# Kernel optimization log

Hardware: AMD Instinct MI355X
Metric: run time of the kernel (lower is better)

Reference implementation:

```python
import jax, jax.numpy as jnp
import numpy as np
from jax import lax

FEAT_STRIDE = 16
BOX_SIZES = (4.0, 8.0, 12.0, 16.0, 24.0, 32.0, 48.0, 64.0, 96.0)
SCALE = 1.0
NUM_ANCHORS = 9
MIN_SIZE = 3.0          # rpn_config.MIN_SIZE (feature-map units)
NMS_THRESH = 0.7        # rpn_config.NMS_THRESH
PRE_NMS_TOP_N = 6000    # rpn_config.PRE_NMS_TOP_N
POST_NMS_TOP_N = 300    # rpn_config.POST_NMS_TOP_N


def _generate_anchors(H, W):
    # [A,H,W,4] boxes in (x, y, w, h); coord 0 pairs with the height axis,
    # matching clip_boxes_batch which clips index 0/2 against `length`=height.
    s = jnp.asarray(BOX_SIZES, jnp.float32) * SCALE                  # [A]
    cy = jnp.arange(H, dtype=jnp.float32) + 0.5
    cx = jnp.arange(W, dtype=jnp.float32) + 0.5
    shp = (NUM_ANCHORS, H, W)
    x0 = jnp.broadcast_to(cy[None, :, None] - s[:, None, None] / 2, shp)
    y0 = jnp.broadcast_to(cx[None, None, :] - s[:, None, None] / 2, shp)
    wh = jnp.broadcast_to(s[:, None, None], shp)
    return jnp.stack([x0, y0, wh, wh], axis=-1)


def _clip_boxes(boxes, H, W):
    # Faithful to clip_boxes_batch: clamp all entries at 0, convert to corners,
    # clamp x against height, y against width, convert back to (x,y,w,h).
    b = jnp.maximum(boxes, 0.0)
    x1, y1, w, h = b[..., 0], b[..., 1], b[..., 2], b[..., 3]
    x2, y2 = x1 + w, y1 + h
    x1 = jnp.minimum(x1, H)
    y1 = jnp.minimum(y1, W)
    x2 = jnp.minimum(x2, H)
    y2 = jnp.minimum(y2, W)
    return jnp.stack([x1, y1, x2 - x1, y2 - y1], axis=-1)


def setup_inputs() -> dict:
    key = jax.random.key(0)
    k1, k2 = jax.random.split(key)
    scores = jax.random.uniform(k1, (1, NUM_ANCHORS, 128, 128), dtype=jnp.float32)
    bbox_deltas = jax.random.normal(k2, (1, 4 * NUM_ANCHORS, 128, 128), dtype=jnp.float32)
    image_metadata = jnp.zeros((1, 3), dtype=jnp.float32)  # unused by forward
    return {"scores": scores, "bbox_deltas": bbox_deltas, "image_metadata": image_metadata}


def reference(scores, bbox_deltas, image_metadata):
    b, A, H, W = scores.shape
    anchors = _generate_anchors(H, W)[None]                 # [1,A,H,W,4]
    # torch view chain (A*4,H,W)->(A,4,H,W)->(A,H,W,4) over contiguous memory
    # is a single reshape of the flat buffer:
    deltas = bbox_deltas.reshape(b, A, H, W, 4)
    boxes = _clip_boxes(anchors + deltas, float(H), float(W))
    flat = boxes.reshape(-1, 4)                             # [N,4], N=A*H*W
    keep = (flat[:, 2] >= MIN_SIZE) & (flat[:, 3] >= MIN_SIZE)
    sc = jnp.where(keep, scores.reshape(-1), -jnp.inf)      # mask instead of compaction (jit-safe)
    _, top = lax.top_k(sc, PRE_NMS_TOP_N)                   # score-descending pre-NMS top-N
    props = flat[top]                                       # [K,4]

    # --- greedy NMS, processing order = descending y2 (as in source `nms`) ---
    x1, y1, w, h = props[:, 0], props[:, 1], props[:, 2], props[:, 3]
    x2, y2 = x1 + w, y1 + h
    order = jnp.argsort(-y2)
    x1, y1, x2, y2 = x1[order], y1[order], x2[order], y2[order]
    area = jnp.maximum((x2 - x1) * (y2 - y1), 1e-6)         # areas = l*b in source
    iw = jnp.maximum(jnp.minimum(x2[:, None], x2[None, :]) - jnp.maximum(x1[:, None], x1[None, :]) + 1.0, 0.0)
    ih = jnp.maximum(jnp.minimum(y2[:, None], y2[None, :]) - jnp.maximum(y1[:, None], y1[None, :]) + 1.0, 0.0)
    ov = iw * ih / area[None, :]                            # intersection / area[j], as in source

    K = PRE_NMS_TOP_N

    def body(valid, i):
        supp = (ov[i] >= NMS_THRESH) & valid
        supp = supp.at[i].set(False)
        return jnp.where(valid[i], valid & ~supp, valid), None

    valid, _ = lax.scan(body, jnp.ones((K,), bool), jnp.arange(K))

    # kept boxes first, in processing order; pad with zeros to POST_NMS_TOP_N
    perm = jnp.argsort(jnp.where(valid, jnp.arange(K), K))
    sel = perm[:POST_NMS_TOP_N]
    out = props[order][sel] * valid[sel][:, None].astype(props.dtype)
    return out[None]                                        # [1, POST_NMS_TOP_N, 4]
```

## Files before the change

### kernel.cpp

```cpp
#include <hip/hip_runtime.h>
#include <cstdint>
#include <cstddef>

#define N_TOT   147456
#define K_PRE   6000
#define K_POST  300
#define CAP     32768
#define MW      188
#define ROWS_PAD 6144
#define CH      256
#define NCH     24
#define CT      128
#define ROWB    24
#define COLB    47
#define G       16

__constant__ float c_sizes[9] = {4.f,8.f,12.f,16.f,24.f,32.f,48.f,64.f,96.f};

__device__ uint32_t g_hist[4096];
__device__ uint32_t g_cnt;

__device__ __forceinline__ void compute_box(int idx, const float* __restrict__ deltas,
                                            float& px1, float& py1, float& pw, float& ph) {
    int a   = idx >> 14;
    int rem = idx & 16383;
    int h   = rem >> 7;
    int w   = rem & 127;
    float s    = c_sizes[a];
    float half = s * 0.5f;
    const float4 d = *(const float4*)(deltas + (size_t)a * 65536 + (size_t)rem * 4);
    float b0 = (((float)h + 0.5f) - half) + d.x;
    float b1 = (((float)w + 0.5f) - half) + d.y;
    float b2 = s + d.z;
    float b3 = s + d.w;
    b0 = fmaxf(b0, 0.0f); b1 = fmaxf(b1, 0.0f);
    b2 = fmaxf(b2, 0.0f); b3 = fmaxf(b3, 0.0f);
    float x1 = b0, y1 = b1;
    float x2 = b0 + b2, y2 = b1 + b3;
    x1 = fminf(x1, 128.0f); y1 = fminf(y1, 128.0f);
    x2 = fminf(x2, 128.0f); y2 = fminf(y2, 128.0f);
    px1 = x1; py1 = y1; pw = x2 - x1; ph = y2 - y1;
}

__device__ __forceinline__ uint32_t waveReduceSum(uint32_t v) {
    #pragma unroll
    for (int o = 32; o > 0; o >>= 1) v += __shfl_xor(v, o, 64);
    return v;
}

__global__ void k_keys_hist(const float* __restrict__ scores, const float* __restrict__ deltas,
                            uint32_t* __restrict__ keys) {
    __shared__ uint32_t lh[4096];
    for (int i = threadIdx.x; i < 4096; i += 256) lh[i] = 0u;
    __syncthreads();
    int t4 = (blockIdx.x * 256 + threadIdx.x) * 4;
    float4 sc4 = *(const float4*)(scores + t4);
    uint32_t k4[4];
    #pragma unroll
    for (int e = 0; e < 4; e++) {
        int idx = t4 + e;
        float px1, py1, pw, ph;
        compute_box(idx, deltas, px1, py1, pw, ph);
        bool keep = (pw >= 3.0f) && (ph >= 3.0f);
        float sc = (&sc4.x)[e];
        uint32_t key = keep ? __float_as_uint(sc) : 0u;
        k4[e] = key;
        atomicAdd(&lh[key >> 20], 1u);
    }
    *(uint4*)(keys + t4) = make_uint4(k4[0], k4[1], k4[2], k4[3]);
    __syncthreads();
    for (int i = threadIdx.x; i < 4096; i += 256) {
        uint32_t v = lh[i];
        if (v) atomicAdd(&g_hist[i], v);
    }
}

__global__ void k_findbin_compact(const uint32_t* __restrict__ keys,
                                  uint64_t* __restrict__ cand) {
    __shared__ uint32_t lh[4096];
    __shared__ uint32_t seg[256];
    __shared__ uint32_t bsh;
    __shared__ uint32_t lcnt, lbase;
    if (threadIdx.x == 0) lcnt = 0u;
    for (int i = threadIdx.x; i < 4096; i += 256) lh[i] = g_hist[i];
    __syncthreads();
    uint32_t s = 0;
    #pragma unroll
    for (int q = 0; q < 16; q++) s += lh[threadIdx.x * 16 + q];
    seg[threadIdx.x] = s;
    __syncthreads();
    for (int off = 1; off < 256; off <<= 1) {
        uint32_t v = seg[threadIdx.x];
        if (threadIdx.x + off < 256) v += seg[threadIdx.x + off];
        __syncthreads();
        seg[threadIdx.x] = v;
        __syncthreads();
    }
    uint32_t St  = seg[threadIdx.x];
    uint32_t St1 = (threadIdx.x < 255) ? seg[threadIdx.x + 1] : 0u;
    if (St >= K_PRE && St1 < K_PRE) {
        uint32_t c2 = St1;
        uint32_t bstar = 0u;
        for (int q = 15; q >= 0; q--) {
            c2 += lh[threadIdx.x * 16 + q];
            if (c2 >= K_PRE) { bstar = (uint32_t)(threadIdx.x * 16 + q); break; }
        }
        bsh = bstar;
    }
    if (threadIdx.x == 0 && seg[0] < K_PRE) bsh = 0u;
    __syncthreads();
    uint32_t bstar = bsh;
    int t4 = (blockIdx.x * 256 + threadIdx.x) * 4;
    uint4 kk = *(const uint4*)(keys + t4);
    bool s0 = (kk.x >> 20) >= bstar;
    bool s1 = (kk.y >> 20) >= bstar;
    bool s2 = (kk.z >> 20) >= bstar;
    bool s3 = (kk.w >> 20) >= bstar;
    uint32_t nsel = (uint32_t)s0 + s1 + s2 + s3;
    uint32_t myoff = 0u;
    if (nsel) myoff = atomicAdd(&lcnt, nsel);
    __syncthreads();
    if (threadIdx.x == 0) lbase = atomicAdd(&g_cnt, lcnt);
    __syncthreads();
    uint32_t pos = lbase + myoff;
    if (s0) { if (pos < CAP) cand[pos] = ((uint64_t)kk.x << 32) | (uint32_t)(~(uint32_t)(t4 + 0)); pos++; }
    if (s1) { if (pos < CAP) cand[pos] = ((uint64_t)kk.y << 32) | (uint32_t)(~(uint32_t)(t4 + 1)); pos++; }
    if (s2) { if (pos < CAP) cand[pos] = ((uint64_t)kk.z << 32) | (uint32_t)(~(uint32_t)(t4 + 2)); pos++; }
    if (s3) { if (pos < CAP) cand[pos] = ((uint64_t)kk.w << 32) | (uint32_t)(~(uint32_t)(t4 + 3)); }
}

__global__ void __launch_bounds__(256) k_rank_props(
        const uint64_t* __restrict__ cand,
        const float* __restrict__ deltas,
        float4* __restrict__ P, uint64_t* __restrict__ yk) {
    __shared__ uint32_t part[4][G];
    uint32_t C = g_cnt;
    if (C > CAP) C = CAP;
    uint32_t nGroups = (C + G - 1) / G;
    int tid  = threadIdx.x;
    int wave = tid >> 6, lane = tid & 63;
    for (uint32_t g = blockIdx.x; g < nGroups; g += gridDim.x) {
        uint32_t b = g * G;
        uint64_t m[G];
        uint32_t cnt[G];
        #pragma unroll
        for (int q = 0; q < G; q++) {
            m[q] = (b + q < C) ? cand[b + q] : ~0ull;
            cnt[q] = 0u;
        }
        for (uint32_t j0 = 0; j0 < C; j0 += 1024) {
            uint32_t ja = j0 + tid, jb = ja + 256, jc = ja + 512, jd = ja + 768;
            uint64_t ka = (ja < C) ? cand[ja] : 0ull;
            uint64_t kb = (jb < C) ? cand[jb] : 0ull;
            uint64_t kc = (jc < C) ? cand[jc] : 0ull;
            uint64_t kd = (jd < C) ? cand[jd] : 0ull;
            #pragma unroll
            for (int q = 0; q < G; q++)
                cnt[q] += (uint32_t)(ka > m[q]) + (uint32_t)(kb > m[q])
                        + (uint32_t)(kc > m[q]) + (uint32_t)(kd > m[q]);
        }
        #pragma unroll
        for (int q = 0; q < G; q++) cnt[q] = waveReduceSum(cnt[q]);
        if (lane == 0) {
            #pragma unroll
            for (int q = 0; q < G; q++) part[wave][q] = cnt[q];
        }
        __syncthreads();
        if (tid < G && b + tid < C) {
            uint32_t r = part[0][tid] + part[1][tid] + part[2][tid] + part[3][tid];
            if (r < K_PRE) {
                int idx = (int)(~((uint32_t)cand[b + tid]));
                float px1, py1, pw, ph;
                compute_box(idx, deltas, px1, py1, pw, ph);
                P[r] = make_float4(px1, py1, pw, ph);
                float y2 = py1 + ph;
                yk[r] = ((uint64_t)__float_as_uint(y2) << 32) | (uint32_t)(~r);
            }
        }
        __syncthreads();
    }
}

__global__ void __launch_bounds__(256) k_rank_y2(
        const uint64_t* __restrict__ ykey, const float4* __restrict__ P,
        float4* __restrict__ OP, float4* __restrict__ Q, float* __restrict__ Bnd) {
    __shared__ uint32_t part[4][G];
    int tid  = threadIdx.x;
    int wave = tid >> 6, lane = tid & 63;
    uint32_t b = blockIdx.x * G;
    uint64_t m[G];
    uint32_t cnt[G];
    #pragma unroll
    for (int q = 0; q < G; q++) {
        m[q] = ykey[b + q];
        cnt[q] = 0u;
    }
    for (uint32_t j0 = 0; j0 < K_PRE; j0 += 1024) {
        uint32_t ja = j0 + tid, jb = ja + 256, jc = ja + 512, jd = ja + 768;
        uint64_t ka = (ja < K_PRE) ? ykey[ja] : 0ull;
        uint64_t kb = (jb < K_PRE) ? ykey[jb] : 0ull;
        uint64_t kc = (jc < K_PRE) ? ykey[jc] : 0ull;
        uint64_t kd = (jd < K_PRE) ? ykey[jd] : 0ull;
        #pragma unroll
        for (int q = 0; q < G; q++)
            cnt[q] += (uint32_t)(ka > m[q]) + (uint32_t)(kb > m[q])
                    + (uint32_t)(kc > m[q]) + (uint32_t)(kd > m[q]);
    }
    #pragma unroll
    for (int q = 0; q < G; q++) cnt[q] = waveReduceSum(cnt[q]);
    if (lane == 0) {
        #pragma unroll
        for (int q = 0; q < G; q++) part[wave][q] = cnt[q];
    }
    __syncthreads();
    if (tid < G) {
        uint32_t r = part[0][tid] + part[1][tid] + part[2][tid] + part[3][tid];
        float4 p = P[b + tid];
        OP[r] = p;
        float x1 = p.x, y1 = p.y;
        float x2 = x1 + p.z, y2 = y1 + p.w;
        float area = fmaxf((x2 - x1) * (y2 - y1), 1e-6f);
        Q[r] = make_float4(x1, y1, x2, y2);
        const double Mc = (double)0.7f - 0x1.0p-25;
        double c = Mc * (double)area;
        float Bf = (float)c;
        if (!((double)Bf > c)) Bf = __int_as_float(__float_as_int(Bf) + 1);
        Bnd[r] = Bf;
    }
}

__global__ void __launch_bounds__(256) k_mask(const float4* __restrict__ Q,
                                              const float* __restrict__ Bnd,
                                              uint32_t* __restrict__ mask) {
    __shared__ float4 qs[CT];
    __shared__ float  bs[CT];
    int i  = blockIdx.x * 256 + threadIdx.x;
    int c0 = blockIdx.y * CT;
    int ncols = min(CT, K_PRE - c0);
    bool rowok = (i < K_PRE);
    float4 qi = rowok ? Q[i] : make_float4(0.f, 0.f, 0.f, 0.f);
    for (int j = threadIdx.x; j < ncols; j += 256) {
        qs[j] = Q[c0 + j];
        bs[j] = Bnd[c0 + j];
    }
    __syncthreads();
    int nw = (ncols + 31) >> 5;
    for (int w = 0; w < nw; w++) {
        uint32_t bits = 0u;
        int jb = w * 32;
        int jn = min(32, ncols - jb);
        #pragma unroll 8
        for (int b = 0; b < jn; b++) {
            int j = jb + b;
            float4 qj = qs[j];
            float iw = fminf(qi.z, qj.z) - fmaxf(qi.x, qj.x) + 1.0f;
            iw = fmaxf(iw, 0.0f);
            float ih = fminf(qi.w, qj.w) - fmaxf(qi.y, qj.y) + 1.0f;
            ih = fmaxf(ih, 0.0f);
            float d = iw * ih;
            bits |= (d >= bs[j]) ? (1u << b) : 0u;
        }
        if (rowok) {
            int gj = c0 + jb;
            uint32_t selfo = (uint32_t)(i - gj);
            if (selfo < 32u) bits &= ~(1u << selfo);
            mask[(size_t)i * MW + (gj >> 5)] = bits;
        }
    }
}

__global__ void __launch_bounds__(256) k_scan(const uint32_t* __restrict__ mask,
                                              const float4* __restrict__ OP,
                                              float* __restrict__ out) {
    __shared__ uint32_t rem[192];
    __shared__ uint32_t sidx[CH];
    __shared__ uint32_t svL[192];
    __shared__ uint32_t nsSh;
    __shared__ uint32_t pref[MW];
    int tid = threadIdx.x;
    if (tid < 16) {
        #pragma unroll
        for (int q = 0; q < 16; q++) g_hist[tid * 16 + q] = 0u;
    }
    if (tid == 16) g_cnt = 0u;
    if (tid < 192) { rem[tid] = 0u; svL[tid] = 0u; }
    for (int i = tid; i < K_POST * 4; i += 256) out[i] = 0.0f;
    __syncthreads();
    uint4 s00 = make_uint4(0,0,0,0), s01 = s00, s10 = s00, s11 = s00;
    uint4 s20 = s00, s21 = s00, s30 = s00, s31 = s00;
    if (tid < 64) {
        const uint32_t* p0 = mask + (size_t)(tid) * MW;
        s00 = *(const uint4*)p0;       s01 = *(const uint4*)(p0 + 4);
        const uint32_t* p1 = mask + (size_t)(64 + tid) * MW;
        s10 = *(const uint4*)p1;       s11 = *(const uint4*)(p1 + 4);
        const uint32_t* p2 = mask + (size_t)(128 + tid) * MW;
        s20 = *(const uint4*)p2;       s21 = *(const uint4*)(p2 + 4);
        const uint32_t* p3 = mask + (size_t)(192 + tid) * MW;
        s30 = *(const uint4*)p3;       s31 = *(const uint4*)(p3 + 4);
    }
    for (int c = 0; c < NCH; c++) {
        int base = c * CH;
        if (tid < 64) {
            uint64_t w0 = ~(((uint64_t)rem[8*c+1] << 32) | (uint64_t)rem[8*c+0]);
            uint64_t w1 = ~(((uint64_t)rem[8*c+3] << 32) | (uint64_t)rem[8*c+2]);
            uint64_t w2 = ~(((uint64_t)rem[8*c+5] << 32) | (uint64_t)rem[8*c+4]);
            uint64_t w3 = ~(((uint64_t)rem[8*c+7] << 32) | (uint64_t)rem[8*c+6]);
            int rows = K_PRE - base;
            if (rows < CH) {
                auto msk = [](int v) -> uint64_t {
                    return v <= 0 ? 0ull : (v >= 64 ? ~0ull : ((1ull << v) - 1ull));
                };
                w0 &= msk(rows); w1 &= msk(rows - 64);
                w2 &= msk(rows - 128); w3 &= msk(rows - 192);
            }
            uint64_t sv0 = 0ull, sv1 = 0ull, sv2 = 0ull, sv3 = 0ull;
            while (w0 | w1 | w2 | w3) {
                int k;
                uint32_t a0, a1, a2, a3, a4, a5, a6, a7;
                if (w0) {
                    k = __ffsll((unsigned long long)w0) - 1;
                    sv0 |= 1ull << k; w0 &= ~(1ull << k);
                    a0 = (uint32_t)__builtin_amdgcn_readlane((int)s00.x, k);
                    a1 = (uint32_t)__builtin_amdgcn_readlane((int)s00.y, k);
                    a2 = (uint32_t)__builtin_amdgcn_readlane((int)s00.z, k);
                    a3 = (uint32_t)__builtin_amdgcn_readlane((int)s00.w, k);
                    a4 = (uint32_t)__builtin_amdgcn_readlane((int)s01.x, k);
                    a5 = (uint32_t)__builtin_amdgcn_readlane((int)s01.y, k);
                    a6 = (uint32_t)__builtin_amdgcn_readlane((int)s01.z, k);
                    a7 = (uint32_t)__builtin_amdgcn_readlane((int)s01.w, k);
                } else if (w1) {
                    k = __ffsll((unsigned long long)w1) - 1;
                    sv1 |= 1ull << k; w1 &= ~(1ull << k);
                    a0 = (uint32_t)__builtin_amdgcn_readlane((int)s10.x, k);
                    a1 = (uint32_t)__builtin_amdgcn_readlane((int)s10.y, k);
                    a2 = (uint32_t)__builtin_amdgcn_readlane((int)s10.z, k);
                    a3 = (uint32_t)__builtin_amdgcn_readlane((int)s10.w, k);
                    a4 = (uint32_t)__builtin_amdgcn_readlane((int)s11.x, k);
                    a5 = (uint32_t)__builtin_amdgcn_readlane((int)s11.y, k);
                    a6 = (uint32_t)__builtin_amdgcn_readlane((int)s11.z, k);
                    a7 = (uint32_t)__builtin_amdgcn_readlane((int)s11.w, k);
                } else if (w2) {
                    k = __ffsll((unsigned long long)w2) - 1;
                    sv2 |= 1ull << k; w2 &= ~(1ull << k);
                    a0 = (uint32_t)__builtin_amdgcn_readlane((int)s20.x, k);
                    a1 = (uint32_t)__builtin_amdgcn_readlane((int)s20.y, k);
                    a2 = (uint32_t)__builtin_amdgcn_readlane((int)s20.z, k);
                    a3 = (uint32_t)__builtin_amdgcn_readlane((int)s20.w, k);
                    a4 = (uint32_t)__builtin_amdgcn_readlane((int)s21.x, k);
                    a5 = (uint32_t)__builtin_amdgcn_readlane((int)s21.y, k);
                    a6 = (uint32_t)__builtin_amdgcn_readlane((int)s21.z, k);
                    a7 = (uint32_t)__builtin_amdgcn_readlane((int)s21.w, k);
                } else {
                    k = __ffsll((unsigned long long)w3) - 1;
                    sv3 |= 1ull << k; w3 &= ~(1ull << k);
                    a0 = (uint32_t)__builtin_amdgcn_readlane((int)s30.x, k);
                    a1 = (uint32_t)__builtin_amdgcn_readlane((int)s30.y, k);
                    a2 = (uint32_t)__builtin_amdgcn_readlane((int)s30.z, k);
                    a3 = (uint32_t)__builtin_amdgcn_readlane((int)s30.w, k);
                    a4 = (uint32_t)__builtin_amdgcn_readlane((int)s31.x, k);
                    a5 = (uint32_t)__builtin_amdgcn_readlane((int)s31.y, k);
                    a6 = (uint32_t)__builtin_amdgcn_readlane((int)s31.z, k);
                    a7 = (uint32_t)__builtin_amdgcn_readlane((int)s31.w, k);
                }
                w0 &= ~(((uint64_t)a1 << 32) | (uint64_t)a0);
                w1 &= ~(((uint64_t)a3 << 32) | (uint64_t)a2);
                w2 &= ~(((uint64_t)a5 << 32) | (uint64_t)a4);
                w3 &= ~(((uint64_t)a7 << 32) | (uint64_t)a6);
            }
            uint32_t n0 = (uint32_t)__popcll(sv0), n1 = (uint32_t)__popcll(sv1);
            uint32_t n2 = (uint32_t)__popcll(sv2), n3 = (uint32_t)__popcll(sv3);
            uint32_t o1 = n0, o2 = n0 + n1, o3 = n0 + n1 + n2, ns = o3 + n3;
            if (tid == 0) {
                svL[8*c+0] = (uint32_t)sv0; svL[8*c+1] = (uint32_t)(sv0 >> 32);
                svL[8*c+2] = (uint32_t)sv1; svL[8*c+3] = (uint32_t)(sv1 >> 32);
                svL[8*c+4] = (uint32_t)sv2; svL[8*c+5] = (uint32_t)(sv2 >> 32);
                svL[8*c+6] = (uint32_t)sv3; svL[8*c+7] = (uint32_t)(sv3 >> 32);
                nsSh = ns;
            }
            uint64_t lowm = (1ull << tid) - 1ull;
            if ((sv0 >> tid) & 1ull) sidx[      __popcll(sv0 & lowm)] = (uint32_t)(base + tid);
            if ((sv1 >> tid) & 1ull) sidx[o1 +  __popcll(sv1 & lowm)] = (uint32_t)(base + 64 + tid);
            if ((sv2 >> tid) & 1ull) sidx[o2 +  __popcll(sv2 & lowm)] = (uint32_t)(base + 128 + tid);
            if ((sv3 >> tid) & 1ull) sidx[o3 +  __popcll(sv3 & lowm)] = (uint32_t)(base + 192 + tid);
            if (ns) {
                uint32_t nsPad = (ns + 31u) & ~31u;
                uint32_t first;
                if      (sv0) first = (uint32_t)base +       (uint32_t)(__ffsll((unsigned long long)sv0) - 1);
                else if (sv1) first = (uint32_t)base + 64u + (uint32_t)(__ffsll((unsigned long long)sv1) - 1);
                else if (sv2) first = (uint32_t)base + 128u+ (uint32_t)(__ffsll((unsigned long long)sv2) - 1);
                else          first = (uint32_t)base + 192u+ (uint32_t)(__ffsll((unsigned long long)sv3) - 1);
                #pragma unroll
                for (int rr = 0; rr < 4; rr++) {
                    uint32_t ii = (uint32_t)tid + 64u * rr;
                    if (ii >= ns && ii < nsPad) sidx[ii] = first;
                }
            }
            if (c + 1 < NCH) {
                const uint32_t* p0 = mask + (size_t)(base + 256 + tid) * MW + 8*(c+1);
                s00 = *(const uint4*)p0;  s01 = *(const uint4*)(p0 + 4);
                const uint32_t* p1 = p0 + (size_t)64 * MW;
                s10 = *(const uint4*)p1;  s11 = *(const uint4*)(p1 + 4);
                const uint32_t* p2 = p1 + (size_t)64 * MW;
                s20 = *(const uint4*)p2;  s21 = *(const uint4*)(p2 + 4);
                const uint32_t* p3 = p2 + (size_t)64 * MW;
                s30 = *(const uint4*)p3;  s31 = *(const uint4*)(p3 + 4);
            }
        }
        __syncthreads();
        int w = tid - 64;
        if (w >= 0 && w < MW) {
            uint32_t nsPad = (nsSh + 31u) & ~31u;
            uint32_t acc = rem[w];
            for (uint32_t t2 = 0; t2 < nsPad; t2 += 32) {
                uint32_t r[32];
                #pragma unroll
                for (int q = 0; q < 32; q++)
                    r[q] = mask[(size_t)sidx[t2 + q] * MW + w];
                uint32_t o = 0u;
                #pragma unroll
                for (int q = 0; q < 32; q++) o |= r[q];
                acc |= o;
            }
            rem[w] = acc;
        }
        __syncthreads();
    }
    if (tid < MW) {
        uint32_t vv = svL[tid] & ~rem[tid];
        if (tid == MW - 1) vv &= 0xFFFFu;
        rem[tid] = vv;
    }
    __syncthreads();
    if (tid == 0) {
        uint32_t run = 0;
        for (int w2 = 0; w2 < MW; w2++) { pref[w2] = run; run += (uint32_t)__popc(rem[w2]); }
    }
    __syncthreads();
    if (tid < MW) {
        uint32_t b = rem[tid];
        uint32_t r = pref[tid];
        int basebit = tid * 32;
        while (b && r < K_POST) {
            int bit = __ffs(b) - 1;
            b &= b - 1u;
            float4 pp = OP[basebit + bit];
            *(float4*)(out + (size_t)r * 4) = pp;
            r++;
        }
    }
}

extern "C" void kernel_launch(void* const* d_in, const int* in_sizes, int n_in,
                              void* d_out, int out_size, void* d_ws, size_t ws_size,
                              hipStream_t stream) {
    (void)in_sizes; (void)n_in; (void)out_size; (void)ws_size;
    const float* scores = (const float*)d_in[0];
    const float* deltas = (const float*)d_in[1];
    float* out = (float*)d_out;

    char* ws = (char*)d_ws;
    size_t off = 0;
    auto alloc = [&](size_t bytes) -> void* {
        void* p = ws + off;
        off += (bytes + 255) & ~(size_t)255;
        return p;
    };
    uint32_t* keys  = (uint32_t*)alloc((size_t)N_TOT * 4);
    uint64_t* cand  = (uint64_t*)alloc((size_t)CAP * 8);
    float4*   P     = (float4*)alloc((size_t)K_PRE * 16);
    uint64_t* yk    = (uint64_t*)alloc((size_t)K_PRE * 8);
    float4*   OP    = (float4*)alloc((size_t)K_PRE * 16);
    float4*   Q     = (float4*)alloc((size_t)K_PRE * 16);
    float*    Bnd   = (float*)alloc((size_t)K_PRE * 4);
    uint32_t* mask  = (uint32_t*)alloc((size_t)ROWS_PAD * MW * 4 + 256);

    k_keys_hist<<<N_TOT / 1024, 256, 0, stream>>>(scores, deltas, keys);
    k_findbin_compact<<<N_TOT / 1024, 256, 0, stream>>>(keys, cand);
    k_rank_props<<<1024, 256, 0, stream>>>(cand, deltas, P, yk);
    k_rank_y2<<<K_PRE / G, 256, 0, stream>>>(yk, P, OP, Q, Bnd);
    k_mask<<<dim3(ROWB, COLB), 256, 0, stream>>>(Q, Bnd, mask);
    k_scan<<<1, 256, 0, stream>>>(mask, OP, out);
}
```

Measured before the change: 143.3 us.

## Fuse all six stages into one persistent kernel with grid barriers

Replaces the six separate kernel launches with a single persistent kernel of 576 blocks that runs histogram, compaction, score ranking, y2 ranking, mask building and the serial scan as phases separated by software grid barriers on global atomic counters. The goal is to remove per-launch overhead and the idle gaps between short dependent kernels. In exchange, it requires all 576 blocks to be co-resident, since the spin barriers would otherwise deadlock; the barrier loop has a timeout to guard against this. It also caps each block at 256 threads via launch bounds, and the final scan runs on one block while the others sit idle.

Result: slower. 405.1 us (+182.8%).

```diff
diff --git a/kernel.cpp b/kernel.cpp
--- a/kernel.cpp
+++ b/kernel.cpp
@@ -13,12 +13,42 @@
 #define CT      128
 #define ROWB    24
 #define COLB    47
+#define NTILE   (ROWB*COLB)
 #define G       16
+#define NBLK    576
+#define HBLK    144
+
+#define OFF_KEYS 0u
+#define OFF_CAND 589824u
+#define OFF_P    851968u
+#define OFF_YK   948224u
+#define OFF_OP   996352u
+#define OFF_Q    1092608u
+#define OFF_BND  1188864u
+#define OFF_MASK 1212928u
 
 __constant__ float c_sizes[9] = {4.f,8.f,12.f,16.f,24.f,32.f,48.f,64.f,96.f};
 
 __device__ uint32_t g_hist[4096];
 __device__ uint32_t g_cnt;
+__device__ uint32_t g_bar[8];
+
+__device__ __forceinline__ void gridBarrier(int i) {
+    __syncthreads();
+    if (threadIdx.x == 0) {
+        __threadfence();
+        uint32_t ticket = atomicAdd(&g_bar[i], 1u);
+        uint32_t target = (ticket / NBLK + 1u) * NBLK;
+        uint32_t tries = 0;
+        while (__hip_atomic_load(&g_bar[i], __ATOMIC_RELAXED,
+                                 __HIP_MEMORY_SCOPE_AGENT) < target) {
+            __builtin_amdgcn_s_sleep(2);
+            if (++tries > (1u << 24)) break;
+        }
+        __threadfence();
+    }
+    __syncthreads();
+}
 
 __device__ __forceinline__ void compute_box(int idx, const float* __restrict__ deltas,
                                             float& px1, float& py1, float& pw, float& ph) {
@@ -48,112 +78,171 @@
     return v;
 }
 
-__global__ void k_keys_hist(const float* __restrict__ scores, const float* __restrict__ deltas,
-                            uint32_t* __restrict__ keys) {
-    __shared__ uint32_t lh[4096];
-    for (int i = threadIdx.x; i < 4096; i += 256) lh[i] = 0u;
-    __syncthreads();
-    int t4 = (blockIdx.x * 256 + threadIdx.x) * 4;
-    float4 sc4 = *(const float4*)(scores + t4);
-    uint32_t k4[4];
-    #pragma unroll
-    for (int e = 0; e < 4; e++) {
-        int idx = t4 + e;
-        float px1, py1, pw, ph;
-        compute_box(idx, deltas, px1, py1, pw, ph);
-        bool keep = (pw >= 3.0f) && (ph >= 3.0f);
-        float sc = (&sc4.x)[e];
-        uint32_t key = keep ? __float_as_uint(sc) : 0u;
-        k4[e] = key;
-        atomicAdd(&lh[key >> 20], 1u);
-    }
-    *(uint4*)(keys + t4) = make_uint4(k4[0], k4[1], k4[2], k4[3]);
-    __syncthreads();
-    for (int i = threadIdx.x; i < 4096; i += 256) {
-        uint32_t v = lh[i];
-        if (v) atomicAdd(&g_hist[i], v);
-    }
-}
-
-__global__ void k_findbin_compact(const uint32_t* __restrict__ keys,
-                                  uint64_t* __restrict__ cand) {
-    __shared__ uint32_t lh[4096];
-    __shared__ uint32_t seg[256];
-    __shared__ uint32_t bsh;
-    __shared__ uint32_t lcnt, lbase;
-    if (threadIdx.x == 0) lcnt = 0u;
-    for (int i = threadIdx.x; i < 4096; i += 256) lh[i] = g_hist[i];
-    __syncthreads();
-    uint32_t s = 0;
-    #pragma unroll
-    for (int q = 0; q < 16; q++) s += lh[threadIdx.x * 16 + q];
-    seg[threadIdx.x] = s;
-    __syncthreads();
-    for (int off = 1; off < 256; off <<= 1) {
-        uint32_t v = seg[threadIdx.x];
-        if (threadIdx.x + off < 256) v += seg[threadIdx.x + off];
-        __syncthreads();
-        seg[threadIdx.x] = v;
-        __syncthreads();
-    }
-    uint32_t St  = seg[threadIdx.x];
-    uint32_t St1 = (threadIdx.x < 255) ? seg[threadIdx.x + 1] : 0u;
-    if (St >= K_PRE && St1 < K_PRE) {
-        uint32_t c2 = St1;
-        uint32_t bstar = 0u;
-        for (int q = 15; q >= 0; q--) {
-            c2 += lh[threadIdx.x * 16 + q];
-            if (c2 >= K_PRE) { bstar = (uint32_t)(threadIdx.x * 16 + q); break; }
-        }
-        bsh = bstar;
-    }
-    if (threadIdx.x == 0 && seg[0] < K_PRE) bsh = 0u;
-    __syncthreads();
-    uint32_t bstar = bsh;
-    int t4 = (blockIdx.x * 256 + threadIdx.x) * 4;
-    uint4 kk = *(const uint4*)(keys + t4);
-    bool s0 = (kk.x >> 20) >= bstar;
-    bool s1 = (kk.y >> 20) >= bstar;
-    bool s2 = (kk.z >> 20) >= bstar;
-    bool s3 = (kk.w >> 20) >= bstar;
-    uint32_t nsel = (uint32_t)s0 + s1 + s2 + s3;
-    uint32_t myoff = 0u;
-    if (nsel) myoff = atomicAdd(&lcnt, nsel);
-    __syncthreads();
-    if (threadIdx.x == 0) lbase = atomicAdd(&g_cnt, lcnt);
-    __syncthreads();
-    uint32_t pos = lbase + myoff;
-    if (s0) { if (pos < CAP) cand[pos] = ((uint64_t)kk.x << 32) | (uint32_t)(~(uint32_t)(t4 + 0)); pos++; }
-    if (s1) { if (pos < CAP) cand[pos] = ((uint64_t)kk.y << 32) | (uint32_t)(~(uint32_t)(t4 + 1)); pos++; }
-    if (s2) { if (pos < CAP) cand[pos] = ((uint64_t)kk.z << 32) | (uint32_t)(~(uint32_t)(t4 + 2)); pos++; }
-    if (s3) { if (pos < CAP) cand[pos] = ((uint64_t)kk.w << 32) | (uint32_t)(~(uint32_t)(t4 + 3)); }
-}
-
-__global__ void __launch_bounds__(256) k_rank_props(
-        const uint64_t* __restrict__ cand,
-        const float* __restrict__ deltas,
-        float4* __restrict__ P, uint64_t* __restrict__ yk) {
-    __shared__ uint32_t part[4][G];
-    uint32_t C = g_cnt;
-    if (C > CAP) C = CAP;
-    uint32_t nGroups = (C + G - 1) / G;
-    int tid  = threadIdx.x;
-    int wave = tid >> 6, lane = tid & 63;
-    for (uint32_t g = blockIdx.x; g < nGroups; g += gridDim.x) {
-        uint32_t b = g * G;
+__global__ void __launch_bounds__(256, 4) mega(const float* __restrict__ scores,
+                                               const float* __restrict__ deltas,
+                                               float* __restrict__ out,
+                                               char* __restrict__ ws) {
+    __shared__ __align__(16) char smem[17664];
+
+    uint32_t* keys = (uint32_t*)(ws + OFF_KEYS);
+    uint64_t* cand = (uint64_t*)(ws + OFF_CAND);
+    float4*   P    = (float4*)(ws + OFF_P);
+    uint64_t* yk   = (uint64_t*)(ws + OFF_YK);
+    float4*   OP   = (float4*)(ws + OFF_OP);
+    float4*   Q    = (float4*)(ws + OFF_Q);
+    float*    Bnd  = (float*)(ws + OFF_BND);
+    uint32_t* mask = (uint32_t*)(ws + OFF_MASK);
+
+    const int tid  = threadIdx.x;
+    const int bid  = blockIdx.x;
+    const int wave = tid >> 6, lane = tid & 63;
+
+    if (bid < HBLK) {
+        uint32_t* lh = (uint32_t*)smem;
+        for (int i = tid; i < 4096; i += 256) lh[i] = 0u;
+        __syncthreads();
+        int t4 = (bid * 256 + tid) * 4;
+        float4 sc4 = *(const float4*)(scores + t4);
+        uint32_t k4[4];
+        #pragma unroll
+        for (int e = 0; e < 4; e++) {
+            int idx = t4 + e;
+            float px1, py1, pw, ph;
+            compute_box(idx, deltas, px1, py1, pw, ph);
+            bool keep = (pw >= 3.0f) && (ph >= 3.0f);
+            float sc = (&sc4.x)[e];
+            uint32_t key = keep ? __float_as_uint(sc) : 0u;
+            k4[e] = key;
+            atomicAdd(&lh[key >> 20], 1u);
+        }
+        *(uint4*)(keys + t4) = make_uint4(k4[0], k4[1], k4[2], k4[3]);
+        __syncthreads();
+        for (int i = tid; i < 4096; i += 256) {
+            uint32_t v = lh[i];
+            if (v) atomicAdd(&g_hist[i], v);
+        }
+    }
+    gridBarrier(0);
+
+    if (bid < HBLK) {
+        uint32_t* lh   = (uint32_t*)smem;
+        uint32_t* seg  = (uint32_t*)(smem + 16384);
+        uint32_t* bshp = (uint32_t*)(smem + 16384 + 1024);
+        uint32_t* lcnt = bshp + 1;
+        uint32_t* lbas = bshp + 2;
+        if (tid == 0) lcnt[0] = 0u;
+        for (int i = tid; i < 4096; i += 256) lh[i] = g_hist[i];
+        __syncthreads();
+        uint32_t s = 0;
+        #pragma unroll
+        for (int q = 0; q < 16; q++) s += lh[tid * 16 + q];
+        seg[tid] = s;
+        __syncthreads();
+        for (int off = 1; off < 256; off <<= 1) {
+            uint32_t v = seg[tid];
+            if (tid + off < 256) v += seg[tid + off];
+            __syncthreads();
+            seg[tid] = v;
+            __syncthreads();
+        }
+        uint32_t St  = seg[tid];
+        uint32_t St1 = (tid < 255) ? seg[tid + 1] : 0u;
+        if (St >= K_PRE && St1 < K_PRE) {
+            uint32_t c2 = St1;
+            uint32_t bstar = 0u;
+            for (int q = 15; q >= 0; q--) {
+                c2 += lh[tid * 16 + q];
+                if (c2 >= K_PRE) { bstar = (uint32_t)(tid * 16 + q); break; }
+            }
+            bshp[0] = bstar;
+        }
+        if (tid == 0 && seg[0] < K_PRE) bshp[0] = 0u;
+        __syncthreads();
+        uint32_t bstar = bshp[0];
+        int t4 = (bid * 256 + tid) * 4;
+        uint4 kk = *(const uint4*)(keys + t4);
+        bool s0 = (kk.x >> 20) >= bstar;
+        bool s1 = (kk.y >> 20) >= bstar;
+        bool s2 = (kk.z >> 20) >= bstar;
+        bool s3 = (kk.w >> 20) >= bstar;
+        uint32_t nsel = (uint32_t)s0 + s1 + s2 + s3;
+        uint32_t myoff = 0u;
+        if (nsel) myoff = atomicAdd(lcnt, nsel);
+        __syncthreads();
+        if (tid == 0) lbas[0] = atomicAdd(&g_cnt, lcnt[0]);
+        __syncthreads();
+        uint32_t pos = lbas[0] + myoff;
+        if (s0) { if (pos < CAP) cand[pos] = ((uint64_t)kk.x << 32) | (uint32_t)(~(uint32_t)(t4 + 0)); pos++; }
+        if (s1) { if (pos < CAP) cand[pos] = ((uint64_t)kk.y << 32) | (uint32_t)(~(uint32_t)(t4 + 1)); pos++; }
+        if (s2) { if (pos < CAP) cand[pos] = ((uint64_t)kk.z << 32) | (uint32_t)(~(uint32_t)(t4 + 2)); pos++; }
+        if (s3) { if (pos < CAP) cand[pos] = ((uint64_t)kk.w << 32) | (uint32_t)(~(uint32_t)(t4 + 3)); }
+    }
+    gridBarrier(1);
+
+    {
+        uint32_t (*part)[G] = (uint32_t (*)[G])smem;
+        uint32_t C = g_cnt;
+        if (C > CAP) C = CAP;
+        uint32_t nGroups = (C + G - 1) / G;
+        for (uint32_t g = bid; g < nGroups; g += NBLK) {
+            uint32_t b = g * G;
+            uint64_t m[G];
+            uint32_t cnt[G];
+            #pragma unroll
+            for (int q = 0; q < G; q++) {
+                m[q] = (b + q < C) ? cand[b + q] : ~0ull;
+                cnt[q] = 0u;
+            }
+            for (uint32_t j0 = 0; j0 < C; j0 += 1024) {
+                uint32_t ja = j0 + tid, jb = ja + 256, jc = ja + 512, jd = ja + 768;
+                uint64_t ka = (ja < C) ? cand[ja] : 0ull;
+                uint64_t kb = (jb < C) ? cand[jb] : 0ull;
+                uint64_t kc = (jc < C) ? cand[jc] : 0ull;
+                uint64_t kd = (jd < C) ? cand[jd] : 0ull;
+                #pragma unroll
+                for (int q = 0; q < G; q++)
+                    cnt[q] += (uint32_t)(ka > m[q]) + (uint32_t)(kb > m[q])
+                            + (uint32_t)(kc > m[q]) + (uint32_t)(kd > m[q]);
+            }
+            #pragma unroll
+            for (int q = 0; q < G; q++) cnt[q] = waveReduceSum(cnt[q]);
+            if (lane == 0) {
+                #pragma unroll
+                for (int q = 0; q < G; q++) part[wave][q] = cnt[q];
+            }
+            __syncthreads();
+            if (tid < G && b + tid < C) {
+                uint32_t r = part[0][tid] + part[1][tid] + part[2][tid] + part[3][tid];
+                if (r < K_PRE) {
+                    int idx = (int)(~((uint32_t)cand[b + tid]));
+                    float px1, py1, pw, ph;
+                    compute_box(idx, deltas, px1, py1, pw, ph);
+                    P[r] = make_float4(px1, py1, pw, ph);
+                    float y2 = py1 + ph;
+                    yk[r] = ((uint64_t)__float_as_uint(y2) << 32) | (uint32_t)(~r);
+                }
+            }
+            __syncthreads();
+        }
+    }
+    gridBarrier(2);
+
+    if (bid < K_PRE / G) {
+        uint32_t (*part)[G] = (uint32_t (*)[G])smem;
+        uint32_t b = (uint32_t)bid * G;
         uint64_t m[G];
         uint32_t cnt[G];
         #pragma unroll
         for (int q = 0; q < G; q++) {
-            m[q] = (b + q < C) ? cand[b + q] : ~0ull;
+            m[q] = yk[b + q];
             cnt[q] = 0u;
         }
-        for (uint32_t j0 = 0; j0 < C; j0 += 1024) {
+        for (uint32_t j0 = 0; j0 < K_PRE; j0 += 1024) {
             uint32_t ja = j0 + tid, jb = ja + 256, jc = ja + 512, jd = ja + 768;
-            uint64_t ka = (ja < C) ? cand[ja] : 0ull;
-            uint64_t kb = (jb < C) ? cand[jb] : 0ull;
-            uint64_t kc = (jc < C) ? cand[jc] : 0ull;
-            uint64_t kd = (jd < C) ? cand[jd] : 0ull;
+            uint64_t ka = (ja < K_PRE) ? yk[ja] : 0ull;
+            uint64_t kb = (jb < K_PRE) ? yk[jb] : 0ull;
+            uint64_t kc = (jc < K_PRE) ? yk[jc] : 0ull;
+            uint64_t kd = (jd < K_PRE) ? yk[jd] : 0ull;
             #pragma unroll
             for (int q = 0; q < G; q++)
                 cnt[q] += (uint32_t)(ka > m[q]) + (uint32_t)(kb > m[q])
@@ -166,286 +255,243 @@
             for (int q = 0; q < G; q++) part[wave][q] = cnt[q];
         }
         __syncthreads();
-        if (tid < G && b + tid < C) {
+        if (tid < G) {
             uint32_t r = part[0][tid] + part[1][tid] + part[2][tid] + part[3][tid];
-            if (r < K_PRE) {
-                int idx = (int)(~((uint32_t)cand[b + tid]));
-                float px1, py1, pw, ph;
-                compute_box(idx, deltas, px1, py1, pw, ph);
-                P[r] = make_float4(px1, py1, pw, ph);
-                float y2 = py1 + ph;
-                yk[r] = ((uint64_t)__float_as_uint(y2) << 32) | (uint32_t)(~r);
-            }
-        }
-        __syncthreads();
-    }
-}
-
-__global__ void __launch_bounds__(256) k_rank_y2(
-        const uint64_t* __restrict__ ykey, const float4* __restrict__ P,
-        float4* __restrict__ OP, float4* __restrict__ Q, float* __restrict__ Bnd) {
-    __shared__ uint32_t part[4][G];
-    int tid  = threadIdx.x;
-    int wave = tid >> 6, lane = tid & 63;
-    uint32_t b = blockIdx.x * G;
-    uint64_t m[G];
-    uint32_t cnt[G];
-    #pragma unroll
-    for (int q = 0; q < G; q++) {
-        m[q] = ykey[b + q];
-        cnt[q] = 0u;
-    }
-    for (uint32_t j0 = 0; j0 < K_PRE; j0 += 1024) {
-        uint32_t ja = j0 + tid, jb = ja + 256, jc = ja + 512, jd = ja + 768;
-        uint64_t ka = (ja < K_PRE) ? ykey[ja] : 0ull;
-        uint64_t kb = (jb < K_PRE) ? ykey[jb] : 0ull;
-        uint64_t kc = (jc < K_PRE) ? ykey[jc] : 0ull;
-        uint64_t kd = (jd < K_PRE) ? ykey[jd] : 0ull;
-        #pragma unroll
-        for (int q = 0; q < G; q++)
-            cnt[q] += (uint32_t)(ka > m[q]) + (uint32_t)(kb > m[q])
-                    + (uint32_t)(kc > m[q]) + (uint32_t)(kd > m[q]);
-    }
-    #pragma unroll
-    for (int q = 0; q < G; q++) cnt[q] = waveReduceSum(cnt[q]);
-    if (lane == 0) {
-        #pragma unroll
-        for (int q = 0; q < G; q++) part[wave][q] = cnt[q];
-    }
-    __syncthreads();
-    if (tid < G) {
-        uint32_t r = part[0][tid] + part[1][tid] + part[2][tid] + part[3][tid];
-        float4 p = P[b + tid];
-        OP[r] = p;
-        float x1 = p.x, y1 = p.y;
-        float x2 = x1 + p.z, y2 = y1 + p.w;
-        float area = fmaxf((x2 - x1) * (y2 - y1), 1e-6f);
-        Q[r] = make_float4(x1, y1, x2, y2);
-        const double Mc = (double)0.7f - 0x1.0p-25;
-        double c = Mc * (double)area;
-        float Bf = (float)c;
-        if (!((double)Bf > c)) Bf = __int_as_float(__float_as_int(Bf) + 1);
-        Bnd[r] = Bf;
-    }
-}
-
-__global__ void __launch_bounds__(256) k_mask(const float4* __restrict__ Q,
-                                              const float* __restrict__ Bnd,
-                                              uint32_t* __restrict__ mask) {
-    __shared__ float4 qs[CT];
-    __shared__ float  bs[CT];
-    int i  = blockIdx.x * 256 + threadIdx.x;
-    int c0 = blockIdx.y * CT;
-    int ncols = min(CT, K_PRE - c0);
-    bool rowok = (i < K_PRE);
-    float4 qi = rowok ? Q[i] : make_float4(0.f, 0.f, 0.f, 0.f);
-    for (int j = threadIdx.x; j < ncols; j += 256) {
-        qs[j] = Q[c0 + j];
-        bs[j] = Bnd[c0 + j];
-    }
-    __syncthreads();
-    int nw = (ncols + 31) >> 5;
-    for (int w = 0; w < nw; w++) {
-        uint32_t bits = 0u;
-        int jb = w * 32;
-        int jn = min(32, ncols - jb);
-        #pragma unroll 8
-        for (int b = 0; b < jn; b++) {
-            int j = jb + b;
-            float4 qj = qs[j];
-            float iw = fminf(qi.z, qj.z) - fmaxf(qi.x, qj.x) + 1.0f;
-            iw = fmaxf(iw, 0.0f);
-            float ih = fminf(qi.w, qj.w) - fmaxf(qi.y, qj.y) + 1.0f;
-            ih = fmaxf(ih, 0.0f);
-            float d = iw * ih;
-            bits |= (d >= bs[j]) ? (1u << b) : 0u;
-        }
-        if (rowok) {
-            int gj = c0 + jb;
-            uint32_t selfo = (uint32_t)(i - gj);
-            if (selfo < 32u) bits &= ~(1u << selfo);
-            mask[(size_t)i * MW + (gj >> 5)] = bits;
-        }
-    }
-}
-
-__global__ void __launch_bounds__(256) k_scan(const uint32_t* __restrict__ mask,
-                                              const float4* __restrict__ OP,
-                                              float* __restrict__ out) {
-    __shared__ uint32_t rem[192];
-    __shared__ uint32_t sidx[CH];
-    __shared__ uint32_t svL[192];
-    __shared__ uint32_t nsSh;
-    __shared__ uint32_t pref[MW];
-    int tid = threadIdx.x;
-    if (tid < 16) {
-        #pragma unroll
-        for (int q = 0; q < 16; q++) g_hist[tid * 16 + q] = 0u;
-    }
-    if (tid == 16) g_cnt = 0u;
-    if (tid < 192) { rem[tid] = 0u; svL[tid] = 0u; }
-    for (int i = tid; i < K_POST * 4; i += 256) out[i] = 0.0f;
-    __syncthreads();
-    uint4 s00 = make_uint4(0,0,0,0), s01 = s00, s10 = s00, s11 = s00;
-    uint4 s20 = s00, s21 = s00, s30 = s00, s31 = s00;
-    if (tid < 64) {
-        const uint32_t* p0 = mask + (size_t)(tid) * MW;
-        s00 = *(const uint4*)p0;       s01 = *(const uint4*)(p0 + 4);
-        const uint32_t* p1 = mask + (size_t)(64 + tid) * MW;
-        s10 = *(const uint4*)p1;       s11 = *(const uint4*)(p1 + 4);
-        const uint32_t* p2 = mask + (size_t)(128 + tid) * MW;
-        s20 = *(const uint4*)p2;       s21 = *(const uint4*)(p2 + 4);
-        const uint32_t* p3 = mask + (size_t)(192 + tid) * MW;
-        s30 = *(const uint4*)p3;       s31 = *(const uint4*)(p3 + 4);
-    }
-    for (int c = 0; c < NCH; c++) {
-        int base = c * CH;
+            float4 p = P[b + tid];
+            OP[r] = p;
+            float x1 = p.x, y1 = p.y;
+            float x2 = x1 + p.z, y2 = y1 + p.w;
+            float area = fmaxf((x2 - x1) * (y2 - y1), 1e-6f);
+            Q[r] = make_float4(x1, y1, x2, y2);
+            const double Mc = (double)0.7f - 0x1.0p-25;
+            double c = Mc * (double)area;
+            float Bf = (float)c;
+            if (!((double)Bf > c)) Bf = __int_as_float(__float_as_int(Bf) + 1);
+            Bnd[r] = Bf;
+        }
+    }
+    gridBarrier(3);
+
+    {
+        float4* qs = (float4*)smem;
+        float*  bs = (float*)(smem + CT * 16);
+        for (uint32_t t = bid; t < NTILE; t += NBLK) {
+            int bx = (int)(t % ROWB);
+            int by = (int)(t / ROWB);
+            int i  = bx * 256 + tid;
+            int c0 = by * CT;
+            int ncols = min(CT, K_PRE - c0);
+            bool rowok = (i < K_PRE);
+            float4 qi = rowok ? Q[i] : make_float4(0.f, 0.f, 0.f, 0.f);
+            __syncthreads();
+            for (int j = tid; j < ncols; j += 256) {
+                qs[j] = Q[c0 + j];
+                bs[j] = Bnd[c0 + j];
+            }
+            __syncthreads();
+            int nw = (ncols + 31) >> 5;
+            for (int w = 0; w < nw; w++) {
+                uint32_t bits = 0u;
+                int jb = w * 32;
+                int jn = min(32, ncols - jb);
+                #pragma unroll 8
+                for (int b = 0; b < jn; b++) {
+                    int j = jb + b;
+                    float4 qj = qs[j];
+                    float iw = fminf(qi.z, qj.z) - fmaxf(qi.x, qj.x) + 1.0f;
+                    iw = fmaxf(iw, 0.0f);
+                    float ih = fminf(qi.w, qj.w) - fmaxf(qi.y, qj.y) + 1.0f;
+                    ih = fmaxf(ih, 0.0f);
+                    float d = iw * ih;
+                    bits |= (d >= bs[j]) ? (1u << b) : 0u;
+                }
+                if (rowok) {
+                    int gj = c0 + jb;
+                    uint32_t selfo = (uint32_t)(i - gj);
+                    if (selfo < 32u) bits &= ~(1u << selfo);
+                    mask[(size_t)i * MW + (gj >> 5)] = bits;
+                }
+            }
+        }
+    }
+    gridBarrier(4);
+    if (bid != 0) return;
+
+    {
+        uint32_t* rem  = (uint32_t*)smem;
+        uint32_t* sidx = rem + 192;
+        uint32_t* svL  = sidx + CH;
+        uint32_t* pref = svL + 192;
+        uint32_t* nsSh = pref + MW;
+        if (tid < 16) {
+            #pragma unroll
+            for (int q = 0; q < 16; q++) g_hist[tid * 16 + q] = 0u;
+        }
+        if (tid == 16) g_cnt = 0u;
+        if (tid < 192) { rem[tid] = 0u; svL[tid] = 0u; }
+        for (int i = tid; i < K_POST * 4; i += 256) out[i] = 0.0f;
+        __syncthreads();
+        uint4 s00 = make_uint4(0,0,0,0), s01 = s00, s10 = s00, s11 = s00;
+        uint4 s20 = s00, s21 = s00, s30 = s00, s31 = s00;
         if (tid < 64) {
-            uint64_t w0 = ~(((uint64_t)rem[8*c+1] << 32) | (uint64_t)rem[8*c+0]);
-            uint64_t w1 = ~(((uint64_t)rem[8*c+3] << 32) | (uint64_t)rem[8*c+2]);
-            uint64_t w2 = ~(((uint64_t)rem[8*c+5] << 32) | (uint64_t)rem[8*c+4]);
-            uint64_t w3 = ~(((uint64_t)rem[8*c+7] << 32) | (uint64_t)rem[8*c+6]);
-            int rows = K_PRE - base;
-            if (rows < CH) {
-                auto msk = [](int v) -> uint64_t {
-                    return v <= 0 ? 0ull : (v >= 64 ? ~0ull : ((1ull << v) - 1ull));
-                };
-                w0 &= msk(rows); w1 &= msk(rows - 64);
-                w2 &= msk(rows - 128); w3 &= msk(rows - 192);
-            }
-            uint64_t sv0 = 0ull, sv1 = 0ull, sv2 = 0ull, sv3 = 0ull;
-            while (w0 | w1 | w2 | w3) {
-                int k;
-                uint32_t a0, a1, a2, a3, a4, a5, a6, a7;
-                if (w0) {
-                    k = __ffsll((unsigned long long)w0) - 1;
-                    sv0 |= 1ull << k; w0 &= ~(1ull << k);
-                    a0 = (uint32_t)__builtin_amdgcn_readlane((int)s00.x, k);
-                    a1 = (uint32_t)__builtin_amdgcn_readlane((int)s00.y, k);
-                    a2 = (uint32_t)__builtin_amdgcn_readlane((int)s00.z, k);
-                    a3 = (uint32_t)__builtin_amdgcn_readlane((int)s00.w, k);
-                    a4 = (uint32_t)__builtin_amdgcn_readlane((int)s01.x, k);
-                    a5 = (uint32_t)__builtin_amdgcn_readlane((int)s01.y, k);
-                    a6 = (uint32_t)__builtin_amdgcn_readlane((int)s01.z, k);
-                    a7 = (uint32_t)__builtin_amdgcn_readlane((int)s01.w, k);
-                } else if (w1) {
-                    k = __ffsll((unsigned long long)w1) - 1;
-                    sv1 |= 1ull << k; w1 &= ~(1ull << k);
-                    a0 = (uint32_t)__builtin_amdgcn_readlane((int)s10.x, k);
-                    a1 = (uint32_t)__builtin_amdgcn_readlane((int)s10.y, k);
-                    a2 = (uint32_t)__builtin_amdgcn_readlane((int)s10.z, k);
-                    a3 = (uint32_t)__builtin_amdgcn_readlane((int)s10.w, k);
-                    a4 = (uint32_t)__builtin_amdgcn_readlane((int)s11.x, k);
-                    a5 = (uint32_t)__builtin_amdgcn_readlane((int)s11.y, k);
-                    a6 = (uint32_t)__builtin_amdgcn_readlane((int)s11.z, k);
-                    a7 = (uint32_t)__builtin_amdgcn_readlane((int)s11.w, k);
-                } else if (w2) {
-                    k = __ffsll((unsigned long long)w2) - 1;
-                    sv2 |= 1ull << k; w2 &= ~(1ull << k);
-                    a0 = (uint32_t)__builtin_amdgcn_readlane((int)s20.x, k);
-                    a1 = (uint32_t)__builtin_amdgcn_readlane((int)s20.y, k);
-                    a2 = (uint32_t)__builtin_amdgcn_readlane((int)s20.z, k);
-                    a3 = (uint32_t)__builtin_amdgcn_readlane((int)s20.w, k);
-                    a4 = (uint32_t)__builtin_amdgcn_readlane((int)s21.x, k);
-                    a5 = (uint32_t)__builtin_amdgcn_readlane((int)s21.y, k);
-                    a6 = (uint32_t)__builtin_amdgcn_readlane((int)s21.z, k);
-                    a7 = (uint32_t)__builtin_amdgcn_readlane((int)s21.w, k);
-                } else {
-                    k = __ffsll((unsigned long long)w3) - 1;
-                    sv3 |= 1ull << k; w3 &= ~(1ull << k);
-                    a0 = (uint32_t)__builtin_amdgcn_readlane((int)s30.x, k);
-                    a1 = (uint32_t)__builtin_amdgcn_readlane((int)s30.y, k);
-                    a2 = (uint32_t)__builtin_amdgcn_readlane((int)s30.z, k);
-                    a3 = (uint32_t)__builtin_amdgcn_readlane((int)s30.w, k);
-                    a4 = (uint32_t)__builtin_amdgcn_readlane((int)s31.x, k);
-                    a5 = (uint32_t)__builtin_amdgcn_readlane((int)s31.y, k);
-                    a6 = (uint32_t)__builtin_amdgcn_readlane((int)s31.z, k);
-                    a7 = (uint32_t)__builtin_amdgcn_readlane((int)s31.w, k);
-                }
-                w0 &= ~(((uint64_t)a1 << 32) | (uint64_t)a0);
-                w1 &= ~(((uint64_t)a3 << 32) | (uint64_t)a2);
-                w2 &= ~(((uint64_t)a5 << 32) | (uint64_t)a4);
-                w3 &= ~(((uint64_t)a7 << 32) | (uint64_t)a6);
-            }
-            uint32_t n0 = (uint32_t)__popcll(sv0), n1 = (uint32_t)__popcll(sv1);
-            uint32_t n2 = (uint32_t)__popcll(sv2), n3 = (uint32_t)__popcll(sv3);
-            uint32_t o1 = n0, o2 = n0 + n1, o3 = n0 + n1 + n2, ns = o3 + n3;
-            if (tid == 0) {
-                svL[8*c+0] = (uint32_t)sv0; svL[8*c+1] = (uint32_t)(sv0 >> 32);
-                svL[8*c+2] = (uint32_t)sv1; svL[8*c+3] = (uint32_t)(sv1 >> 32);
-                svL[8*c+4] = (uint32_t)sv2; svL[8*c+5] = (uint32_t)(sv2 >> 32);
-                svL[8*c+6] = (uint32_t)sv3; svL[8*c+7] = (uint32_t)(sv3 >> 32);
-                nsSh = ns;
-            }
-            uint64_t lowm = (1ull << tid) - 1ull;
-            if ((sv0 >> tid) & 1ull) sidx[      __popcll(sv0 & lowm)] = (uint32_t)(base + tid);
-            if ((sv1 >> tid) & 1ull) sidx[o1 +  __popcll(sv1 & lowm)] = (uint32_t)(base + 64 + tid);
-            if ((sv2 >> tid) & 1ull) sidx[o2 +  __popcll(sv2 & lowm)] = (uint32_t)(base + 128 + tid);
-            if ((sv3 >> tid) & 1ull) sidx[o3 +  __popcll(sv3 & lowm)] = (uint32_t)(base + 192 + tid);
-            if (ns) {
-                uint32_t nsPad = (ns + 31u) & ~31u;
-                uint32_t first;
-                if      (sv0) first = (uint32_t)base +       (uint32_t)(__ffsll((unsigned long long)sv0) - 1);
-                else if (sv1) first = (uint32_t)base + 64u + (uint32_t)(__ffsll((unsigned long long)sv1) - 1);
-                else if (sv2) first = (uint32_t)base + 128u+ (uint32_t)(__ffsll((unsigned long long)sv2) - 1);
-                else          first = (uint32_t)base + 192u+ (uint32_t)(__ffsll((unsigned long long)sv3) - 1);
-                #pragma unroll
-                for (int rr = 0; rr < 4; rr++) {
-                    uint32_t ii = (uint32_t)tid + 64u * rr;
-                    if (ii >= ns && ii < nsPad) sidx[ii] = first;
-                }
-            }
-            if (c + 1 < NCH) {
-                const uint32_t* p0 = mask + (size_t)(base + 256 + tid) * MW + 8*(c+1);
-                s00 = *(const uint4*)p0;  s01 = *(const uint4*)(p0 + 4);
-                const uint32_t* p1 = p0 + (size_t)64 * MW;
-                s10 = *(const uint4*)p1;  s11 = *(const uint4*)(p1 + 4);
-                const uint32_t* p2 = p1 + (size_t)64 * MW;
-                s20 = *(const uint4*)p2;  s21 = *(const uint4*)(p2 + 4);
-                const uint32_t* p3 = p2 + (size_t)64 * MW;
-                s30 = *(const uint4*)p3;  s31 = *(const uint4*)(p3 + 4);
-            }
-        }
-        __syncthreads();
-        int w = tid - 64;
-        if (w >= 0 && w < MW) {
-            uint32_t nsPad = (nsSh + 31u) & ~31u;
-            uint32_t acc = rem[w];
-            for (uint32_t t2 = 0; t2 < nsPad; t2 += 32) {
-                uint32_t r[32];
-                #pragma unroll
-                for (int q = 0; q < 32; q++)
-                    r[q] = mask[(size_t)sidx[t2 + q] * MW + w];
-                uint32_t o = 0u;
-                #pragma unroll
-                for (int q = 0; q < 32; q++) o |= r[q];
-                acc |= o;
-            }
-            rem[w] = acc;
-        }
-        __syncthreads();
-    }
-    if (tid < MW) {
-        uint32_t vv = svL[tid] & ~rem[tid];
-        if (tid == MW - 1) vv &= 0xFFFFu;
-        rem[tid] = vv;
-    }
-    __syncthreads();
-    if (tid == 0) {
-        uint32_t run = 0;
-        for (int w2 = 0; w2 < MW; w2++) { pref[w2] = run; run += (uint32_t)__popc(rem[w2]); }
-    }
-    __syncthreads();
-    if (tid < MW) {
-        uint32_t b = rem[tid];
-        uint32_t r = pref[tid];
-        int basebit = tid * 32;
-        while (b && r < K_POST) {
-            int bit = __ffs(b) - 1;
-            b &= b - 1u;
-            float4 pp = OP[basebit + bit];
-            *(float4*)(out + (size_t)r * 4) = pp;
-            r++;
+            const uint32_t* p0 = mask + (size_t)(tid) * MW;
+            s00 = *(const uint4*)p0;       s01 = *(const uint4*)(p0 + 4);
+            const uint32_t* p1 = mask + (size_t)(64 + tid) * MW;
+            s10 = *(const uint4*)p1;       s11 = *(const uint4*)(p1 + 4);
+            const uint32_t* p2 = mask + (size_t)(128 + tid) * MW;
+            s20 = *(const uint4*)p2;       s21 = *(const uint4*)(p2 + 4);
+            const uint32_t* p3 = mask + (size_t)(192 + tid) * MW;
+            s30 = *(const uint4*)p3;       s31 = *(const uint4*)(p3 + 4);
+        }
+        for (int c = 0; c < NCH; c++) {
+            int base = c * CH;
+            if (tid < 64) {
+                uint64_t w0 = ~(((uint64_t)rem[8*c+1] << 32) | (uint64_t)rem[8*c+0]);
+                uint64_t w1 = ~(((uint64_t)rem[8*c+3] << 32) | (uint64_t)rem[8*c+2]);
+                uint64_t w2 = ~(((uint64_t)rem[8*c+5] << 32) | (uint64_t)rem[8*c+4]);
+                uint64_t w3 = ~(((uint64_t)rem[8*c+7] << 32) | (uint64_t)rem[8*c+6]);
+                int rows = K_PRE - base;
+                if (rows < CH) {
+                    auto msk = [](int v) -> uint64_t {
+                        return v <= 0 ? 0ull : (v >= 64 ? ~0ull : ((1ull << v) - 1ull));
+                    };
+                    w0 &= msk(rows); w1 &= msk(rows - 64);
+                    w2 &= msk(rows - 128); w3 &= msk(rows - 192);
+                }
+                uint64_t sv0 = 0ull, sv1 = 0ull, sv2 = 0ull, sv3 = 0ull;
+                while (w0 | w1 | w2 | w3) {
+                    int k;
+                    uint32_t a0, a1, a2, a3, a4, a5, a6, a7;
+                    if (w0) {
+                        k = __ffsll((unsigned long long)w0) - 1;
+                        sv0 |= 1ull << k; w0 &= ~(1ull << k);
+                        a0 = (uint32_t)__builtin_amdgcn_readlane((int)s00.x, k);
+                        a1 = (uint32_t)__builtin_amdgcn_readlane((int)s00.y, k);
+                        a2 = (uint32_t)__builtin_amdgcn_readlane((int)s00.z, k);
+                        a3 = (uint32_t)__builtin_amdgcn_readlane((int)s00.w, k);
+                        a4 = (uint32_t)__builtin_amdgcn_readlane((int)s01.x, k);
+                        a5 = (uint32_t)__builtin_amdgcn_readlane((int)s01.y, k);
+                        a6 = (uint32_t)__builtin_amdgcn_readlane((int)s01.z, k);
+                        a7 = (uint32_t)__builtin_amdgcn_readlane((int)s01.w, k);
+                    } else if (w1) {
+                        k = __ffsll((unsigned long long)w1) - 1;
+                        sv1 |= 1ull << k; w1 &= ~(1ull << k);
+                        a0 = (uint32_t)__builtin_amdgcn_readlane((int)s10.x, k);
+                        a1 = (uint32_t)__builtin_amdgcn_readlane((int)s10.y, k);
+                        a2 = (uint32_t)__builtin_amdgcn_readlane((int)s10.z, k);
+                        a3 = (uint32_t)__builtin_amdgcn_readlane((int)s10.w, k);
+                        a4 = (uint32_t)__builtin_amdgcn_readlane((int)s11.x, k);
+                        a5 = (uint32_t)__builtin_amdgcn_readlane((int)s11.y, k);
+                        a6 = (uint32_t)__builtin_amdgcn_readlane((int)s11.z, k);
+                        a7 = (uint32_t)__builtin_amdgcn_readlane((int)s11.w, k);
+                    } else if (w2) {
+                        k = __ffsll((unsigned long long)w2) - 1;
+                        sv2 |= 1ull << k; w2 &= ~(1ull << k);
+                        a0 = (uint32_t)__builtin_amdgcn_readlane((int)s20.x, k);
+                        a1 = (uint32_t)__builtin_amdgcn_readlane((int)s20.y, k);
+                        a2 = (uint32_t)__builtin_amdgcn_readlane((int)s20.z, k);
+                        a3 = (uint32_t)__builtin_amdgcn_readlane((int)s20.w, k);
+                        a4 = (uint32_t)__builtin_amdgcn_readlane((int)s21.x, k);
+                        a5 = (uint32_t)__builtin_amdgcn_readlane((int)s21.y, k);
+                        a6 = (uint32_t)__builtin_amdgcn_readlane((int)s21.z, k);
+                        a7 = (uint32_t)__builtin_amdgcn_readlane((int)s21.w, k);
+                    } else {
+                        k = __ffsll((unsigned long long)w3) - 1;
+                        sv3 |= 1ull << k; w3 &= ~(1ull << k);
+                        a0 = (uint32_t)__builtin_amdgcn_readlane((int)s30.x, k);
+                        a1 = (uint32_t)__builtin_amdgcn_readlane((int)s30.y, k);
+                        a2 = (uint32_t)__builtin_amdgcn_readlane((int)s30.z, k);
+                        a3 = (uint32_t)__builtin_amdgcn_readlane((int)s30.w, k);
+                        a4 = (uint32_t)__builtin_amdgcn_readlane((int)s31.x, k);
+                        a5 = (uint32_t)__builtin_amdgcn_readlane((int)s31.y, k);
+                        a6 = (uint32_t)__builtin_amdgcn_readlane((int)s31.z, k);
+                        a7 = (uint32_t)__builtin_amdgcn_readlane((int)s31.w, k);
+                    }
+                    w0 &= ~(((uint64_t)a1 << 32) | (uint64_t)a0);
+                    w1 &= ~(((uint64_t)a3 << 32) | (uint64_t)a2);
+                    w2 &= ~(((uint64_t)a5 << 32) | (uint64_t)a4);
+                    w3 &= ~(((uint64_t)a7 << 32) | (uint64_t)a6);
+                }
+                uint32_t n0 = (uint32_t)__popcll(sv0), n1 = (uint32_t)__popcll(sv1);
+                uint32_t n2 = (uint32_t)__popcll(sv2), n3 = (uint32_t)__popcll(sv3);
+                uint32_t o1 = n0, o2 = n0 + n1, o3 = n0 + n1 + n2, ns = o3 + n3;
+                if (tid == 0) {
+                    svL[8*c+0] = (uint32_t)sv0; svL[8*c+1] = (uint32_t)(sv0 >> 32);
+                    svL[8*c+2] = (uint32_t)sv1; svL[8*c+3] = (uint32_t)(sv1 >> 32);
+                    svL[8*c+4] = (uint32_t)sv2; svL[8*c+5] = (uint32_t)(sv2 >> 32);
+                    svL[8*c+6] = (uint32_t)sv3; svL[8*c+7] = (uint32_t)(sv3 >> 32);
+                    nsSh[0] = ns;
+                }
+                uint64_t lowm = (1ull << tid) - 1ull;
+                if ((sv0 >> tid) & 1ull) sidx[      __popcll(sv0 & lowm)] = (uint32_t)(base + tid);
+                if ((sv1 >> tid) & 1ull) sidx[o1 +  __popcll(sv1 & lowm)] = (uint32_t)(base + 64 + tid);
+                if ((sv2 >> tid) & 1ull) sidx[o2 +  __popcll(sv2 & lowm)] = (uint32_t)(base + 128 + tid);
+                if ((sv3 >> tid) & 1ull) sidx[o3 +  __popcll(sv3 & lowm)] = (uint32_t)(base + 192 + tid);
+                if (ns) {
+                    uint32_t nsPad = (ns + 31u) & ~31u;
+                    uint32_t first;
+                    if      (sv0) first = (uint32_t)base +       (uint32_t)(__ffsll((unsigned long long)sv0) - 1);
+                    else if (sv1) first = (uint32_t)base + 64u + (uint32_t)(__ffsll((unsigned long long)sv1) - 1);
+                    else if (sv2) first = (uint32_t)base + 128u+ (uint32_t)(__ffsll((unsigned long long)sv2) - 1);
+                    else          first = (uint32_t)base + 192u+ (uint32_t)(__ffsll((unsigned long long)sv3) - 1);
+                    #pragma unroll
+                    for (int rr = 0; rr < 4; rr++) {
+                        uint32_t ii = (uint32_t)tid + 64u * rr;
+                        if (ii >= ns && ii < nsPad) sidx[ii] = first;
+                    }
+                }
+                if (c + 1 < NCH) {
+                    const uint32_t* p0 = mask + (size_t)(base + 256 + tid) * MW + 8*(c+1);
+                    s00 = *(const uint4*)p0;  s01 = *(const uint4*)(p0 + 4);
+                    const uint32_t* p1 = p0 + (size_t)64 * MW;
+                    s10 = *(const uint4*)p1;  s11 = *(const uint4*)(p1 + 4);
+                    const uint32_t* p2 = p1 + (size_t)64 * MW;
+                    s20 = *(const uint4*)p2;  s21 = *(const uint4*)(p2 + 4);
+                    const uint32_t* p3 = p2 + (size_t)64 * MW;
+                    s30 = *(const uint4*)p3;  s31 = *(const uint4*)(p3 + 4);
+                }
+            }
+            __syncthreads();
+            int w = tid - 64;
+            if (w >= 0 && w < MW) {
+                uint32_t nsPad = (nsSh[0] + 31u) & ~31u;
+                uint32_t acc = rem[w];
+                for (uint32_t t2 = 0; t2 < nsPad; t2 += 32) {
+                    uint32_t r[32];
+                    #pragma unroll
+                    for (int q = 0; q < 32; q++)
+                        r[q] = mask[(size_t)sidx[t2 + q] * MW + w];
+                    uint32_t o = 0u;
+                    #pragma unroll
+                    for (int q = 0; q < 32; q++) o |= r[q];
+                    acc |= o;
+                }
+                rem[w] = acc;
+            }
+            __syncthreads();
+        }
+        if (tid < MW) {
+            uint32_t vv = svL[tid] & ~rem[tid];
+            if (tid == MW - 1) vv &= 0xFFFFu;
+            rem[tid] = vv;
+        }
+        __syncthreads();
+        if (tid == 0) {
+            uint32_t run = 0;
+            for (int w2 = 0; w2 < MW; w2++) { pref[w2] = run; run += (uint32_t)__popc(rem[w2]); }
+        }
+        __syncthreads();
+        if (tid < MW) {
+            uint32_t b = rem[tid];
+            uint32_t r = pref[tid];
+            int basebit = tid * 32;
+            while (b && r < K_POST) {
+                int bit = __ffs(b) - 1;
+                b &= b - 1u;
+                float4 pp = OP[basebit + bit];
+                *(float4*)(out + (size_t)r * 4) = pp;
+                r++;
+            }
         }
     }
 }
@@ -457,27 +503,6 @@
     const float* scores = (const float*)d_in[0];
     const float* deltas = (const float*)d_in[1];
     float* out = (float*)d_out;
-
     char* ws = (char*)d_ws;
-    size_t off = 0;
-    auto alloc = [&](size_t bytes) -> void* {
-        void* p = ws + off;
-        off += (bytes + 255) & ~(size_t)255;
-        return p;
-    };
-    uint32_t* keys  = (uint32_t*)alloc((size_t)N_TOT * 4);
-    uint64_t* cand  = (uint64_t*)alloc((size_t)CAP * 8);
-    float4*   P     = (float4*)alloc((size_t)K_PRE * 16);
-    uint64_t* yk    = (uint64_t*)alloc((size_t)K_PRE * 8);
-    float4*   OP    = (float4*)alloc((size_t)K_PRE * 16);
-    float4*   Q     = (float4*)alloc((size_t)K_PRE * 16);
-    float*    Bnd   = (float*)alloc((size_t)K_PRE * 4);
-    uint32_t* mask  = (uint32_t*)alloc((size_t)ROWS_PAD * MW * 4 + 256);
-
-    k_keys_hist<<<N_TOT / 1024, 256, 0, stream>>>(scores, deltas, keys);
-    k_findbin_compact<<<N_TOT / 1024, 256, 0, stream>>>(keys, cand);
-    k_rank_props<<<1024, 256, 0, stream>>>(cand, deltas, P, yk);
-    k_rank_y2<<<K_PRE / G, 256, 0, stream>>>(yk, P, OP, Q, Bnd);
-    k_mask<<<dim3(ROWB, COLB), 256, 0, stream>>>(Q, Bnd, mask);
-    k_scan<<<1, 256, 0, stream>>>(mask, OP, out);
+    mega<<<NBLK, 256, 0, stream>>>(scores, deltas, out, ws);
 }
```
